# Optimization experiments

Measured on AMD Instinct MI355X. Metric: run time of the kernel, lower is better.

## Reference

```python
import jax, jax.numpy as jnp
import numpy as np

# dimensions
N = 50000    # nodes
E = 600000   # edges
NS = 64      # scalar (0e) channels of node features
NV = 32      # vector (1o) channels of node features
A = 16       # node attr channels (16x0e)
R = 8        # edge embedding dim (radial basis, 8x0e)
H = 8        # fc_hidden_size
AVG_NB = 12.0  # avg_num_neighbors
# gate layout: NS scalars (silu) + NV gate scalars (sigmoid) gating NV vectors
GS = NS + NV  # 96 scalar channels before gate
NW = NS + NS + NV + NV  # 192 per-edge TP weights (paths: s*Y0->0e, s*Y1->1o, v*Y0->1o, v.Y1->0e)


def setup_inputs() -> dict:
    key = jax.random.key(0)
    ks = jax.random.split(key, 20)
    d = {
        'node_s': jax.random.normal(ks[0], (N, NS), jnp.float32),
        'node_v': jax.random.normal(ks[1], (N, NV, 3), jnp.float32),
        'node_attrs': jax.random.normal(ks[2], (N, A), jnp.float32),
        'edge_emb': jax.random.uniform(ks[3], (E, R), jnp.float32),
        'edge_sh0': jnp.ones((E, 1), jnp.float32),
        'edge_sh1': jax.random.normal(ks[4], (E, 3), jnp.float32),
        'edge_index': jax.random.randint(ks[5], (2, E), 0, N),
        # linear_1 on node feats (per-irrep channel mixing)
        'W1s': jax.random.normal(ks[6], (NS, NS), jnp.float32),
        'W1v': jax.random.normal(ks[7], (NV, NV), jnp.float32),
        # radial MLP producing per-edge TP weights
        'Wm1': jax.random.normal(ks[8], (R, H), jnp.float32),
        'Wm2': jax.random.normal(ks[9], (H, NW), jnp.float32),
        # linear_2: TP out (96x0e+96x1o) -> pre-gate (96x0e+32x1o)
        'W2s': jax.random.normal(ks[10], (GS, GS), jnp.float32),
        'W2v': jax.random.normal(ks[11], (NS + NV, NV), jnp.float32),
        # update UVU TP internal weights (msg x attrs)
        'Wt0': jax.random.normal(ks[12], (NS, A), jnp.float32),
        'Wt1': jax.random.normal(ks[13], (NV, A), jnp.float32),
        # linear_3
        'W3s': jax.random.normal(ks[14], (NS, GS), jnp.float32),
        'W3v': jax.random.normal(ks[15], (NV, NV), jnp.float32),
        # self connection: FullyConnectedTensorProduct(node_feats, attrs -> pre-gate)
        'Wsc0': jax.random.normal(ks[16], (NS, A, GS), jnp.float32),
        'Wsc1': jax.random.normal(ks[17], (NV, A, NV), jnp.float32),
    }
    return d


def _gate(s_all, v):
    # s_all: [.., GS]; first NS scalars -> silu, last NV -> sigmoid gates for vectors
    scal = jax.nn.silu(s_all[..., :NS])
    gates = jax.nn.sigmoid(s_all[..., NS:])
    return scal, v * gates[..., None]


def reference(node_s, node_v, node_attrs, edge_emb, edge_sh0, edge_sh1, edge_index,
              W1s, W1v, Wm1, Wm2, W2s, W2v, Wt0, Wt1, W3s, W3v, Wsc0, Wsc1):
    src, dst = edge_index[0], edge_index[1]

    # ---- message ----
    s1 = (node_s @ W1s) / jnp.sqrt(jnp.float32(NS))                       # [N,NS]
    v1 = jnp.einsum('nuc,uv->nvc', node_v, W1v) / jnp.sqrt(jnp.float32(NV))
    ss = s1[src]   # [E,NS]
    vv = v1[src]   # [E,NV,3]

    # per-edge TP weights from radial MLP
    w = jax.nn.silu(edge_emb @ Wm1) @ Wm2                                 # [E,NW]
    w0a, w1a, w1b, w0b = jnp.split(w, [NS, 2 * NS, 2 * NS + NV], axis=1)

    # UVU tensor product with SH edge attrs (lmax=1)
    t0a = w0a * ss * edge_sh0                                             # [E,NS] 0e
    t0b = w0b * jnp.einsum('euc,ec->eu', vv, edge_sh1)                    # [E,NV] 0e
    t1a = w1a[:, :, None] * ss[:, :, None] * edge_sh1[:, None, :]         # [E,NS,3] 1o
    t1b = w1b[:, :, None] * vv * edge_sh0[:, :, None]                     # [E,NV,3] 1o
    tp_s = jnp.concatenate([t0a, t0b], axis=1)                            # [E,96]
    tp_v = jnp.concatenate([t1a, t1b], axis=1)                            # [E,96,3]

    m_s = (tp_s @ W2s) / jnp.sqrt(jnp.float32(GS))                        # [E,GS]
    m_v = jnp.einsum('euc,uv->evc', tp_v, W2v) / jnp.sqrt(jnp.float32(NS + NV))  # [E,NV,3]
    msg_s, msg_v = _gate(m_s, m_v)                                        # [E,NS], [E,NV,3]

    # ---- update ----
    agg_s = jax.ops.segment_sum(msg_s, dst, num_segments=N) / jnp.sqrt(jnp.float32(AVG_NB))
    agg_v = jax.ops.segment_sum(msg_v, dst, num_segments=N) / jnp.sqrt(jnp.float32(AVG_NB))

    u0 = jnp.einsum('nu,na,ua->nu', agg_s, node_attrs, Wt0) / jnp.sqrt(jnp.float32(A))
    u1 = jnp.einsum('nuc,na,ua->nuc', agg_v, node_attrs, Wt1) / jnp.sqrt(jnp.float32(A))

    f_s = (u0 @ W3s) / jnp.sqrt(jnp.float32(NS))                          # [N,GS]
    f_v = jnp.einsum('nuc,uv->nvc', u1, W3v) / jnp.sqrt(jnp.float32(NV))  # [N,NV,3]

    # self connection (fully connected TP with scalar attrs)
    sc_s = jnp.einsum('nu,na,uav->nv', node_s, node_attrs, Wsc0) / jnp.sqrt(jnp.float32(NS * A))
    sc_v = jnp.einsum('nuc,na,uaw->nwc', node_v, node_attrs, Wsc1) / jnp.sqrt(jnp.float32(NV * A))
    f_s = f_s + sc_s
    f_v = f_v + sc_v

    out_s, out_v = _gate(f_s, f_v)                                        # [N,NS], [N,NV,3]
    return jnp.concatenate([out_s, out_v.reshape(N, NV * 3)], axis=1)     # [N,160]
```

## Files before the change

kernel.cpp:

```cpp
#include <hip/hip_runtime.h>
#include <math.h>

#define N 50000
#define E 600000
#define EPB 16
#define LDK 104

typedef __attribute__((ext_vector_type(8))) short short8;
typedef __attribute__((ext_vector_type(4))) float float4v;

__device__ __forceinline__ float silu_f(float x) { return x / (1.f + __expf(-x)); }
__device__ __forceinline__ float sigm_f(float x) { return 1.f / (1.f + __expf(-x)); }
__device__ __forceinline__ unsigned short f2bf(float f) {
  unsigned u = __float_as_uint(f);
  u += 0x7fff + ((u >> 16) & 1);
  return (unsigned short)(u >> 16);
}
__device__ __forceinline__ float bf2f(unsigned short u) {
  return __uint_as_float(((unsigned)u) << 16);
}

__global__ void k_hist(const int* __restrict__ eidx, int* __restrict__ counts) {
  int e = blockIdx.x * 256 + threadIdx.x;
  if (e < E) atomicAdd(&counts[eidx[E + e]], 1);
}

__global__ __launch_bounds__(1024)
void k_scan(const int* __restrict__ counts, int* __restrict__ row_ptr) {
  __shared__ int ssum[1024];
  const int t = threadIdx.x;
  const int CH = 49;
  int lo = t * CH, hi = min(lo + CH, N);
  int s = 0;
  for (int i = lo; i < hi; i++) s += counts[i];
  ssum[t] = s;
  __syncthreads();
  for (int off = 1; off < 1024; off <<= 1) {
    int v = (t >= off) ? ssum[t - off] : 0;
    __syncthreads();
    ssum[t] += v;
    __syncthreads();
  }
  int run = (t == 0) ? 0 : ssum[t - 1];
  for (int i = lo; i < hi; i++) { row_ptr[i] = run; run += counts[i]; }
  if (t == 1023) row_ptr[N] = ssum[1023];
}

__global__ void k_scatter(const int* __restrict__ eidx, const int* __restrict__ row_ptr,
                          int* __restrict__ woff, int* __restrict__ perm) {
  int e = blockIdx.x * 256 + threadIdx.x;
  if (e < E) {
    int d = eidx[E + e];
    int p = atomicAdd(&woff[d], 1);
    perm[row_ptr[d] + p] = e;
  }
}

__global__ void k_prep(const float* __restrict__ Wsc0, const float* __restrict__ W3s,
                       const float* __restrict__ Wsc1, const float* __restrict__ W3v,
                       const float* __restrict__ W2s, const float* __restrict__ W2v,
                       unsigned short* __restrict__ BT, unsigned short* __restrict__ B2T,
                       unsigned short* __restrict__ w2sTg, unsigned short* __restrict__ w2vTg) {
  const float isq96 = 0.10206207261596575f;
  int i = blockIdx.x * 256 + threadIdx.x;
  if (i < 96 * 1088) {
    int j = i / 1088, k = i % 1088;
    float v;
    if (k < 1024) v = Wsc0[(size_t)k * 96 + j] * 0.03125f;
    else          v = W3s[(size_t)(k - 1024) * 96 + j] * 0.125f;
    BT[i] = f2bf(v);
  } else if (i < 96 * 1088 + 32 * 576) {
    int i2 = i - 96 * 1088;
    int w = i2 / 576, k = i2 % 576;
    float v = 0.f;
    if (k < 512)      v = Wsc1[(size_t)k * 32 + w] * 0.04419417382415922f;
    else if (k < 544) v = W3v[(size_t)(k - 512) * 32 + w] * 0.17677669529663689f;
    B2T[i2] = f2bf(v);
  } else if (i < 96 * 1088 + 32 * 576 + 96 * 96) {
    int i3 = i - (96 * 1088 + 32 * 576);
    int j = i3 / 96, k = i3 % 96;
    w2sTg[i3] = f2bf(W2s[(size_t)k * 96 + j] * isq96);
  } else {
    int i4 = i - (96 * 1088 + 32 * 576 + 96 * 96);
    if (i4 < 32 * 96) {
      int v = i4 / 96, u = i4 % 96;
      w2vTg[i4] = f2bf(W2v[(size_t)u * 32 + v] * isq96);
    }
  }
}

__global__ __launch_bounds__(256, 4)
void k_lin1(const float* __restrict__ node_s, const float* __restrict__ node_v,
            const float* __restrict__ W1s, const float* __restrict__ W1v,
            float* __restrict__ s1, float* __restrict__ v1) {
  __shared__ float w1s[64 * 64];
  __shared__ float w1v[32 * 32];
  for (int i = threadIdx.x; i < 64 * 64; i += 256) w1s[i] = W1s[i];
  for (int i = threadIdx.x; i < 32 * 32; i += 256) w1v[i] = W1v[i];
  __syncthreads();
  const float is_ns = 0.125f;
  const float is_nv = 0.17677669529663689f;
  int gtid = blockIdx.x * 256 + threadIdx.x;
  int stride = gridDim.x * 256;
  for (int i = gtid; i < N * 160; i += stride) {
    int n = i / 160, ch = i % 160;
    if (ch < 64) {
      const float* row = node_s + n * 64;
      float acc = 0.f;
#pragma unroll
      for (int u = 0; u < 64; u++) acc += row[u] * w1s[u * 64 + ch];
      s1[n * 64 + ch] = acc * is_ns;
    } else {
      int p = ch - 64, v = p / 3, c = p % 3;
      const float* row = node_v + n * 96;
      float acc = 0.f;
#pragma unroll
      for (int u = 0; u < 32; u++) acc += row[u * 3 + c] * w1v[u * 32 + v];
      v1[n * 96 + p] = acc * is_nv;
    }
  }
}

template<int STORE>
__global__ __launch_bounds__(256, 4)
void k_msg(const float* __restrict__ s1, const float* __restrict__ v1,
           const float* __restrict__ emb, const float* __restrict__ sh0g,
           const float* __restrict__ sh1g, const int* __restrict__ eidx,
           const float* __restrict__ Wm1, const float* __restrict__ Wm2,
           const unsigned short* __restrict__ w2sTg, const unsigned short* __restrict__ w2vTg,
           float* __restrict__ aggs, float* __restrict__ aggv,
           unsigned short* __restrict__ msgS, unsigned short* __restrict__ msgV) {
  __shared__ float wm2s[192 * 9];
  __shared__ float wm1s[64];
  __shared__ unsigned short tps[EPB * LDK];
  __shared__ unsigned short tpv[EPB * 3 * LDK];
  __shared__ float gat[EPB][33];
  __shared__ float hb[EPB][8];
  __shared__ float sh1b[EPB][4];
  __shared__ float sh0b[EPB];
  __shared__ int ssrc[EPB];
  __shared__ int sdst[EPB];

  const int t = threadIdx.x;
  const int wave = t >> 6, lane = t & 63;
  const int lm = lane & 15, quad = lane >> 4;
  const int subc = t & 15;

  for (int i = t; i < 192 * 8; i += 256) {
    int h = i / 192, c = i % 192;
    wm2s[c * 9 + h] = Wm2[i];
  }
  if (t < 64) wm1s[t] = Wm1[t];

  short8 b1fr[2][3], b2fr[3];
  {
    const int nt0 = wave;
    const int nt1 = (wave + 4 < 6) ? wave + 4 : wave;
    const int nv2 = wave & 1;
#pragma unroll
    for (int kk = 0; kk < 3; kk++) {
      b1fr[0][kk] = *(const short8*)&w2sTg[(nt0 * 16 + lm) * 96 + kk * 32 + quad * 8];
      b1fr[1][kk] = *(const short8*)&w2sTg[(nt1 * 16 + lm) * 96 + kk * 32 + quad * 8];
      b2fr[kk]    = *(const short8*)&w2vTg[(nv2 * 16 + lm) * 96 + kk * 32 + quad * 8];
    }
  }
  __syncthreads();

  for (int pass = blockIdx.x; pass < E / EPB; pass += gridDim.x) {
    const int ebase = pass * EPB;
    __syncthreads();
    if (t < EPB) {
      ssrc[t] = eidx[ebase + t];
      if (!STORE) sdst[t] = eidx[E + ebase + t];
      sh0b[t] = sh0g[ebase + t];
    } else if (t >= 64 && t < 64 + EPB * 3) {
      int i = t - 64;
      sh1b[i / 3][i % 3] = sh1g[ebase * 3 + i];
    } else if (t >= 128) {
      int i = t - 128, el = i >> 3, sub = i & 7;
      float acc = 0.f;
#pragma unroll
      for (int r = 0; r < 8; r++) acc += emb[(ebase + el) * 8 + r] * wm1s[r * 8 + sub];
      hb[el][sub] = silu_f(acc);
    }
    __syncthreads();
    {
      const int el = t >> 4, sub = subc;
      const int src = ssrc[el];
      const float s0v = sh0b[el];
      const float x0 = sh1b[el][0], x1 = sh1b[el][1], x2 = sh1b[el][2];
      float hr[8];
#pragma unroll
      for (int h = 0; h < 8; h++) hr[h] = hb[el][h];
      const float4v ss = *(const float4v*)&s1[(size_t)src * 64 + sub * 4];
      unsigned short tsv[4], tvv[3][4];
#pragma unroll
      for (int i = 0; i < 4; i++) {
        float w0a = 0.f, w1a = 0.f;
#pragma unroll
        for (int h = 0; h < 8; h++) {
          w0a += hr[h] * wm2s[(sub * 4 + i) * 9 + h];
          w1a += hr[h] * wm2s[(64 + sub * 4 + i) * 9 + h];
        }
        const float ssu = ss[i];
        tsv[i] = f2bf(w0a * ssu * s0v);
        const float base = w1a * ssu;
        tvv[0][i] = f2bf(base * x0);
        tvv[1][i] = f2bf(base * x1);
        tvv[2][i] = f2bf(base * x2);
      }
      *(uint2*)&tps[el * LDK + sub * 4] = *(uint2*)tsv;
#pragma unroll
      for (int c = 0; c < 3; c++)
        *(uint2*)&tpv[(el * 3 + c) * LDK + sub * 4] = *(uint2*)tvv[c];
      const float2* vp = (const float2*)&v1[(size_t)src * 96 + sub * 6];
      const float2 va = vp[0], vb = vp[1], vc = vp[2];
      const float v6[6] = {va.x, va.y, vb.x, vb.y, vc.x, vc.y};
      unsigned short ts2[2], tv2[3][2];
#pragma unroll
      for (int i2 = 0; i2 < 2; i2++) {
        float w1b = 0.f, w0b = 0.f;
#pragma unroll
        for (int h = 0; h < 8; h++) {
          w1b += hr[h] * wm2s[(128 + sub * 2 + i2) * 9 + h];
          w0b += hr[h] * wm2s[(160 + sub * 2 + i2) * 9 + h];
        }
        const float vx = v6[i2 * 3 + 0], vy = v6[i2 * 3 + 1], vz = v6[i2 * 3 + 2];
        ts2[i2] = f2bf(w0b * (vx * x0 + vy * x1 + vz * x2));
        tv2[0][i2] = f2bf(w1b * vx * s0v);
        tv2[1][i2] = f2bf(w1b * vy * s0v);
        tv2[2][i2] = f2bf(w1b * vz * s0v);
      }
      *(unsigned*)&tps[el * LDK + 64 + sub * 2] = *(unsigned*)ts2;
#pragma unroll
      for (int c = 0; c < 3; c++)
        *(unsigned*)&tpv[(el * 3 + c) * LDK + 64 + sub * 2] = *(unsigned*)tv2[c];
    }
    __syncthreads();
    {
      short8 afr[3];
#pragma unroll
      for (int kk = 0; kk < 3; kk++)
        afr[kk] = *(const short8*)&tps[lm * LDK + kk * 32 + quad * 8];
#pragma unroll
      for (int t2 = 0; t2 < 2; t2++) {
        const int nt = wave + t2 * 4;
        if (nt < 6) {
          float4v acc = {0.f, 0.f, 0.f, 0.f};
#pragma unroll
          for (int kk = 0; kk < 3; kk++)
            acc = __builtin_amdgcn_mfma_f32_16x16x32_bf16(afr[kk], b1fr[t2][kk], acc, 0, 0, 0);
          const int j = nt * 16 + lm;
#pragma unroll
          for (int reg = 0; reg < 4; reg++) {
            const int e = quad * 4 + reg;
            const float val = acc[reg];
            if (j < 64) {
              if (STORE) msgS[(size_t)(ebase + e) * 64 + j] = f2bf(silu_f(val));
              else atomicAdd(&aggs[(size_t)sdst[e] * 64 + j], silu_f(val));
            } else {
              gat[e][j - 64] = sigm_f(val);
            }
          }
        }
      }
    }
    __syncthreads();
#pragma unroll
    for (int t2 = 0; t2 < 2; t2++) {
      const int tile = wave + t2 * 4;
      if (tile < 6) {
        const int mt = tile >> 1, nt2 = tile & 1;
        float4v acc = {0.f, 0.f, 0.f, 0.f};
#pragma unroll
        for (int kk = 0; kk < 3; kk++) {
          short8 a = *(const short8*)&tpv[(mt * 16 + lm) * LDK + kk * 32 + quad * 8];
          acc = __builtin_amdgcn_mfma_f32_16x16x32_bf16(a, b2fr[kk], acc, 0, 0, 0);
        }
        const int v = nt2 * 16 + lm;
#pragma unroll
        for (int reg = 0; reg < 4; reg++) {
          const int r = mt * 16 + quad * 4 + reg;
          const int e = (r * 171) >> 9, c = r - 3 * e;
          const float val = acc[reg] * gat[e][v];
          if (STORE) msgV[(size_t)(ebase + e) * 96 + v * 3 + c] = f2bf(val);
          else atomicAdd(&aggv[(size_t)sdst[e] * 96 + v * 3 + c], val);
        }
      }
    }
  }
}

__global__ __launch_bounds__(256, 8)
void k_agg(const unsigned short* __restrict__ msgS, const unsigned short* __restrict__ msgV,
           const int* __restrict__ rowp, const int* __restrict__ perm,
           float* __restrict__ aggs, float* __restrict__ aggv) {
  const int wv = threadIdx.x >> 6, lane = threadIdx.x & 63;
  const int n = blockIdx.x * 4 + wv;
  const int lo = rowp[n], hi = rowp[n + 1];
  float sS = 0.f, v0 = 0.f, v1a = 0.f;
  int r = lo;
  for (; r + 2 <= hi; r += 2) {
    const int e0 = perm[r], e1 = perm[r + 1];
    const unsigned short a0 = msgS[(size_t)e0 * 64 + lane];
    const unsigned short a1 = msgS[(size_t)e1 * 64 + lane];
    const unsigned short b0 = msgV[(size_t)e0 * 96 + lane];
    const unsigned short b1 = msgV[(size_t)e1 * 96 + lane];
    unsigned short c0 = 0, c1 = 0;
    if (lane < 32) {
      c0 = msgV[(size_t)e0 * 96 + 64 + lane];
      c1 = msgV[(size_t)e1 * 96 + 64 + lane];
    }
    sS += bf2f(a0) + bf2f(a1);
    v0 += bf2f(b0) + bf2f(b1);
    v1a += bf2f(c0) + bf2f(c1);
  }
  for (; r < hi; r++) {
    const int e0 = perm[r];
    sS += bf2f(msgS[(size_t)e0 * 64 + lane]);
    v0 += bf2f(msgV[(size_t)e0 * 96 + lane]);
    if (lane < 32) v1a += bf2f(msgV[(size_t)e0 * 96 + 64 + lane]);
  }
  aggs[(size_t)n * 64 + lane] = sS;
  aggv[(size_t)n * 96 + lane] = v0;
  if (lane < 32) aggv[(size_t)n * 96 + 64 + lane] = v1a;
}

__global__ __launch_bounds__(256, 4)
void k_c1(const float* __restrict__ node_s, const float* __restrict__ attrs,
          const float* __restrict__ aggs, const float* __restrict__ Wt0,
          const unsigned short* __restrict__ BT,
          float* __restrict__ out, float* __restrict__ gates) {
  __shared__ float s_row[32][64];
  __shared__ float attr[32][16];
  __shared__ float t0[32][64];
  __shared__ float wt0[1024];
  __shared__ unsigned short As[32 * 72];
  const int t = threadIdx.x;
  const int wave = t >> 6, lane = t & 63, lm = lane & 15, quad = lane >> 4;
  const int nbase = blockIdx.x * 32;

  for (int i = t; i < 1024; i += 256) wt0[i] = Wt0[i];
  for (int i = t; i < 2048; i += 256) {
    int nl = i >> 6, u = i & 63, n = nbase + nl;
    s_row[nl][u] = (n < N) ? node_s[(size_t)n * 64 + u] : 0.f;
    t0[nl][u]    = (n < N) ? aggs[(size_t)n * 64 + u] : 0.f;
  }
  for (int i = t; i < 512; i += 256) {
    int nl = i >> 4, a = i & 15, n = nbase + nl;
    attr[nl][a] = (n < N) ? attrs[(size_t)n * 16 + a] : 0.f;
  }
  __syncthreads();
  for (int i = t; i < 2048; i += 256) {
    int nl = i >> 6, u = i & 63;
    float d0 = 0.f;
#pragma unroll
    for (int a = 0; a < 16; a++) d0 += attr[nl][a] * wt0[u * 16 + a];
    t0[nl][u] *= d0 * 0.07216878364870322f;
  }

  float4v acc[3] = {{0,0,0,0},{0,0,0,0},{0,0,0,0}};
  int mts[3], nts[3];
#pragma unroll
  for (int tt = 0; tt < 3; tt++) {
    const int tile = wave + tt * 4;
    mts[tt] = tile / 6;
    nts[tt] = tile % 6;
  }

  for (int kc = 0; kc < 17; kc++) {
    __syncthreads();
    {
      const int row = t >> 3, c0 = (t & 7) * 8;
      unsigned short tmp[8];
      if (kc < 16) {
        const int u = kc * 4 + (c0 >> 4);
        const float sval = s_row[row][u];
        const int ab = c0 & 8;
#pragma unroll
        for (int i = 0; i < 8; i++) tmp[i] = f2bf(sval * attr[row][ab + i]);
      } else {
#pragma unroll
        for (int i = 0; i < 8; i++) tmp[i] = f2bf(t0[row][c0 + i]);
      }
      *(uint4*)&As[row * 72 + c0] = *(uint4*)tmp;
    }
    __syncthreads();
#pragma unroll
    for (int ks = 0; ks < 2; ks++) {
      short8 am0 = *(const short8*)&As[(lm) * 72 + ks * 32 + quad * 8];
      short8 am1 = *(const short8*)&As[(16 + lm) * 72 + ks * 32 + quad * 8];
#pragma unroll
      for (int tt = 0; tt < 3; tt++) {
        short8 b = *(const short8*)&BT[(size_t)(nts[tt] * 16 + lm) * 1088 + kc * 64 + ks * 32 + quad * 8];
        acc[tt] = __builtin_amdgcn_mfma_f32_16x16x32_bf16(mts[tt] ? am1 : am0, b, acc[tt], 0, 0, 0);
      }
    }
  }
#pragma unroll
  for (int tt = 0; tt < 3; tt++) {
    const int j = nts[tt] * 16 + lm;
#pragma unroll
    for (int reg = 0; reg < 4; reg++) {
      const int m = mts[tt] * 16 + quad * 4 + reg;
      const int n = nbase + m;
      if (n < N) {
        const float val = acc[tt][reg];
        if (j < 64) out[(size_t)n * 160 + j] = silu_f(val);
        else        gates[(size_t)n * 32 + (j - 64)] = sigm_f(val);
      }
    }
  }
}

__global__ __launch_bounds__(256, 3)
void k_c2(const float* __restrict__ node_v, const float* __restrict__ attrs,
          const float* __restrict__ aggv, const float* __restrict__ Wt1,
          const unsigned short* __restrict__ B2T, const float* __restrict__ gts,
          float* __restrict__ out) {
  __shared__ float nvs[32][96];
  __shared__ float t1s[32][96];
  __shared__ float attr[32][16];
  __shared__ float wt1[512];
  __shared__ unsigned short As2[96 * 72];
  const int t = threadIdx.x;
  const int wave = t >> 6, lane = t & 63, lm = lane & 15, quad = lane >> 4;
  const int nbase = blockIdx.x * 32;

  for (int i = t; i < 512; i += 256) wt1[i] = Wt1[i];
  for (int i = t; i < 32 * 96; i += 256) {
    int nl = i / 96, rr = i % 96, n = nbase + nl;
    nvs[nl][rr] = (n < N) ? node_v[(size_t)n * 96 + rr] : 0.f;
    t1s[nl][rr] = (n < N) ? aggv[(size_t)n * 96 + rr] : 0.f;
  }
  for (int i = t; i < 512; i += 256) {
    int nl = i >> 4, a = i & 15, n = nbase + nl;
    attr[nl][a] = (n < N) ? attrs[(size_t)n * 16 + a] : 0.f;
  }
  __syncthreads();
  for (int i = t; i < 1024; i += 256) {
    int nl = i >> 5, u = i & 31;
    float d1 = 0.f;
#pragma unroll
    for (int a = 0; a < 16; a++) d1 += attr[nl][a] * wt1[u * 16 + a];
    d1 *= 0.07216878364870322f;
    t1s[nl][u * 3 + 0] *= d1; t1s[nl][u * 3 + 1] *= d1; t1s[nl][u * 3 + 2] *= d1;
  }

  float4v acc[3] = {{0,0,0,0},{0,0,0,0},{0,0,0,0}};
  int mts[3], nts[3];
#pragma unroll
  for (int tt = 0; tt < 3; tt++) {
    const int tile = wave + tt * 4;
    mts[tt] = tile >> 1;
    nts[tt] = tile & 1;
  }

  for (int kc = 0; kc < 9; kc++) {
    __syncthreads();
#pragma unroll
    for (int jj = 0; jj < 3; jj++) {
      const int job = t + jj * 256;
      const int row = job >> 3, c0 = (job & 7) * 8;
      const int nl = (row * 171) >> 9, c = row - 3 * nl;
      const int kbase = kc * 64 + c0;
      unsigned short tmp[8];
      if (kbase < 512) {
        const int u = kbase >> 4;
        const float vval = nvs[nl][u * 3 + c];
        const int ab = c0 & 8;
#pragma unroll
        for (int i = 0; i < 8; i++) tmp[i] = f2bf(vval * attr[nl][ab + i]);
      } else if (kbase < 544) {
        const int u2 = kbase - 512;
#pragma unroll
        for (int i = 0; i < 8; i++) tmp[i] = f2bf(t1s[nl][(u2 + i) * 3 + c]);
      } else {
#pragma unroll
        for (int i = 0; i < 8; i++) tmp[i] = 0;
      }
      *(uint4*)&As2[row * 72 + c0] = *(uint4*)tmp;
    }
    __syncthreads();
#pragma unroll
    for (int ks = 0; ks < 2; ks++) {
#pragma unroll
      for (int tt = 0; tt < 3; tt++) {
        short8 a = *(const short8*)&As2[(mts[tt] * 16 + lm) * 72 + ks * 32 + quad * 8];
        short8 b = *(const short8*)&B2T[(size_t)(nts[tt] * 16 + lm) * 576 + kc * 64 + ks * 32 + quad * 8];
        acc[tt] = __builtin_amdgcn_mfma_f32_16x16x32_bf16(a, b, acc[tt], 0, 0, 0);
      }
    }
  }
#pragma unroll
  for (int tt = 0; tt < 3; tt++) {
    const int w = nts[tt] * 16 + lm;
#pragma unroll
    for (int reg = 0; reg < 4; reg++) {
      const int row = mts[tt] * 16 + quad * 4 + reg;
      const int nl = (row * 171) >> 9, c = row - 3 * nl;
      const int n = nbase + nl;
      if (n < N)
        out[(size_t)n * 160 + 64 + w * 3 + c] = acc[tt][reg] * gts[(size_t)n * 32 + w];
    }
  }
}

extern "C" void kernel_launch(void* const* d_in, const int* in_sizes, int n_in,
                              void* d_out, int out_size, void* d_ws, size_t ws_size,
                              hipStream_t stream) {
  const float* node_s = (const float*)d_in[0];
  const float* node_v = (const float*)d_in[1];
  const float* attrs  = (const float*)d_in[2];
  const float* emb    = (const float*)d_in[3];
  const float* sh0    = (const float*)d_in[4];
  const float* sh1    = (const float*)d_in[5];
  const int*   eidx   = (const int*)d_in[6];
  const float* W1s    = (const float*)d_in[7];
  const float* W1v    = (const float*)d_in[8];
  const float* Wm1    = (const float*)d_in[9];
  const float* Wm2    = (const float*)d_in[10];
  const float* W2s    = (const float*)d_in[11];
  const float* W2v    = (const float*)d_in[12];
  const float* Wt0    = (const float*)d_in[13];
  const float* Wt1    = (const float*)d_in[14];
  const float* W3s    = (const float*)d_in[15];
  const float* W3v    = (const float*)d_in[16];
  const float* Wsc0   = (const float*)d_in[17];
  const float* Wsc1   = (const float*)d_in[18];

  char* p = (char*)d_ws;
  float* s1  = (float*)p;  p += (size_t)N * 64 * 4;
  float* v1f = (float*)p;  p += (size_t)N * 96 * 4;
  float* gts = (float*)p;  p += (size_t)N * 32 * 4;
  unsigned short* BT    = (unsigned short*)p;  p += (size_t)96 * 1088 * 2;
  unsigned short* B2T   = (unsigned short*)p;  p += (size_t)32 * 576 * 2;
  unsigned short* w2sTg = (unsigned short*)p;  p += (size_t)96 * 96 * 2;
  unsigned short* w2vTg = (unsigned short*)p;  p += (size_t)32 * 96 * 2;
  char* pmode = p;
  size_t base = (size_t)(pmode - (char*)d_ws);
  size_t need_store = base + ((size_t)N + 1) * 4 + (size_t)N * 4 + (size_t)N * 4
                    + (size_t)E * 4 + (size_t)E * 64 * 2 + (size_t)E * 96 * 2;
  const bool store = (ws_size >= need_store);

  k_prep<<<528, 256, 0, stream>>>(Wsc0, W3s, Wsc1, W3v, W2s, W2v, BT, B2T, w2sTg, w2vTg);
  k_lin1<<<1024, 256, 0, stream>>>(node_s, node_v, W1s, W1v, s1, v1f);

  if (store) {
    int* rowp = (int*)pmode;
    int* cnt  = rowp + (N + 1);
    int* woff = cnt + N;
    int* perm = woff + N;
    unsigned short* msgS = (unsigned short*)(perm + E);
    unsigned short* msgV = msgS + (size_t)E * 64;
    hipMemsetAsync(cnt, 0, (size_t)N * 2 * 4, stream);
    k_hist<<<(E + 255) / 256, 256, 0, stream>>>(eidx, cnt);
    k_scan<<<1, 1024, 0, stream>>>(cnt, rowp);
    k_scatter<<<(E + 255) / 256, 256, 0, stream>>>(eidx, rowp, woff, perm);
    k_msg<1><<<1536, 256, 0, stream>>>(s1, v1f, emb, sh0, sh1, eidx, Wm1, Wm2,
                                       w2sTg, w2vTg, nullptr, nullptr, msgS, msgV);
    float* aggs = s1;
    float* aggv = v1f;
    k_agg<<<N / 4, 256, 0, stream>>>(msgS, msgV, rowp, perm, aggs, aggv);
    k_c1<<<1563, 256, 0, stream>>>(node_s, attrs, aggs, Wt0, BT, (float*)d_out, gts);
    k_c2<<<1563, 256, 0, stream>>>(node_v, attrs, aggv, Wt1, B2T, gts, (float*)d_out);
  } else {
    float* aggs = (float*)pmode;
    float* aggv = aggs + (size_t)N * 64;
    hipMemsetAsync(aggs, 0, (size_t)N * 160 * 4, stream);
    k_msg<0><<<1536, 256, 0, stream>>>(s1, v1f, emb, sh0, sh1, eidx, Wm1, Wm2,
                                       w2sTg, w2vTg, aggs, aggv, nullptr, nullptr);
    k_c1<<<1563, 256, 0, stream>>>(node_s, attrs, aggs, Wt0, BT, (float*)d_out, gts);
    k_c2<<<1563, 256, 0, stream>>>(node_v, attrs, aggv, Wt1, B2T, gts, (float*)d_out);
  }
}
```

Baseline: 779.3 us.

## Process edges in destination-sorted order so aggregation reads messages contiguously

The message kernel now walks edges through the destination-sorted permutation and writes each message at its sorted position. The aggregation kernel can then read messages sequentially per node instead of gathering through perm. In exchange, the per-edge inputs (src index, sh0, sh1, edge embedding) are now read through an indirection and are gathered rather than streamed. The message kernel grid is also cut from 1536 to 1024 blocks.

```diff
diff --git a/kernel.cpp b/kernel.cpp
--- a/kernel.cpp
+++ b/kernel.cpp
@@ -126,6 +126,7 @@
 void k_msg(const float* __restrict__ s1, const float* __restrict__ v1,
            const float* __restrict__ emb, const float* __restrict__ sh0g,
            const float* __restrict__ sh1g, const int* __restrict__ eidx,
+           const int* __restrict__ perm,
            const float* __restrict__ Wm1, const float* __restrict__ Wm2,
            const unsigned short* __restrict__ w2sTg, const unsigned short* __restrict__ w2vTg,
            float* __restrict__ aggs, float* __restrict__ aggv,
@@ -170,17 +171,21 @@
     const int ebase = pass * EPB;
     __syncthreads();
     if (t < EPB) {
-      ssrc[t] = eidx[ebase + t];
+      const int e = STORE ? perm[ebase + t] : (ebase + t);
+      ssrc[t] = eidx[e];
       if (!STORE) sdst[t] = eidx[E + ebase + t];
-      sh0b[t] = sh0g[ebase + t];
+      sh0b[t] = sh0g[e];
     } else if (t >= 64 && t < 64 + EPB * 3) {
       int i = t - 64;
-      sh1b[i / 3][i % 3] = sh1g[ebase * 3 + i];
+      const int el = i / 3, c = i % 3;
+      const int e = STORE ? perm[ebase + el] : (ebase + el);
+      sh1b[el][c] = sh1g[e * 3 + c];
     } else if (t >= 128) {
       int i = t - 128, el = i >> 3, sub = i & 7;
+      const int e = STORE ? perm[ebase + el] : (ebase + el);
       float acc = 0.f;
 #pragma unroll
-      for (int r = 0; r < 8; r++) acc += emb[(ebase + el) * 8 + r] * wm1s[r * 8 + sub];
+      for (int r = 0; r < 8; r++) acc += emb[e * 8 + r] * wm1s[r * 8 + sub];
       hb[el][sub] = silu_f(acc);
     }
     __syncthreads();
@@ -293,7 +298,7 @@
 
 __global__ __launch_bounds__(256, 8)
 void k_agg(const unsigned short* __restrict__ msgS, const unsigned short* __restrict__ msgV,
-           const int* __restrict__ rowp, const int* __restrict__ perm,
+           const int* __restrict__ rowp,
            float* __restrict__ aggs, float* __restrict__ aggv) {
   const int wv = threadIdx.x >> 6, lane = threadIdx.x & 63;
   const int n = blockIdx.x * 4 + wv;
@@ -301,25 +306,23 @@
   float sS = 0.f, v0 = 0.f, v1a = 0.f;
   int r = lo;
   for (; r + 2 <= hi; r += 2) {
-    const int e0 = perm[r], e1 = perm[r + 1];
-    const unsigned short a0 = msgS[(size_t)e0 * 64 + lane];
-    const unsigned short a1 = msgS[(size_t)e1 * 64 + lane];
-    const unsigned short b0 = msgV[(size_t)e0 * 96 + lane];
-    const unsigned short b1 = msgV[(size_t)e1 * 96 + lane];
+    const unsigned short a0 = msgS[(size_t)r * 64 + lane];
+    const unsigned short a1 = msgS[(size_t)(r + 1) * 64 + lane];
+    const unsigned short b0 = msgV[(size_t)r * 96 + lane];
+    const unsigned short b1 = msgV[(size_t)(r + 1) * 96 + lane];
     unsigned short c0 = 0, c1 = 0;
     if (lane < 32) {
-      c0 = msgV[(size_t)e0 * 96 + 64 + lane];
-      c1 = msgV[(size_t)e1 * 96 + 64 + lane];
+      c0 = msgV[(size_t)r * 96 + 64 + lane];
+      c1 = msgV[(size_t)(r + 1) * 96 + 64 + lane];
     }
     sS += bf2f(a0) + bf2f(a1);
     v0 += bf2f(b0) + bf2f(b1);
     v1a += bf2f(c0) + bf2f(c1);
   }
   for (; r < hi; r++) {
-    const int e0 = perm[r];
-    sS += bf2f(msgS[(size_t)e0 * 64 + lane]);
-    v0 += bf2f(msgV[(size_t)e0 * 96 + lane]);
-    if (lane < 32) v1a += bf2f(msgV[(size_t)e0 * 96 + 64 + lane]);
+    sS += bf2f(msgS[(size_t)r * 64 + lane]);
+    v0 += bf2f(msgV[(size_t)r * 96 + lane]);
+    if (lane < 32) v1a += bf2f(msgV[(size_t)r * 96 + 64 + lane]);
   }
   aggs[(size_t)n * 64 + lane] = sS;
   aggv[(size_t)n * 96 + lane] = v0;
@@ -557,18 +560,18 @@
     k_hist<<<(E + 255) / 256, 256, 0, stream>>>(eidx, cnt);
     k_scan<<<1, 1024, 0, stream>>>(cnt, rowp);
     k_scatter<<<(E + 255) / 256, 256, 0, stream>>>(eidx, rowp, woff, perm);
-    k_msg<1><<<1536, 256, 0, stream>>>(s1, v1f, emb, sh0, sh1, eidx, Wm1, Wm2,
+    k_msg<1><<<1024, 256, 0, stream>>>(s1, v1f, emb, sh0, sh1, eidx, perm, Wm1, Wm2,
                                        w2sTg, w2vTg, nullptr, nullptr, msgS, msgV);
     float* aggs = s1;
     float* aggv = v1f;
-    k_agg<<<N / 4, 256, 0, stream>>>(msgS, msgV, rowp, perm, aggs, aggv);
+    k_agg<<<N / 4, 256, 0, stream>>>(msgS, msgV, rowp, aggs, aggv);
     k_c1<<<1563, 256, 0, stream>>>(node_s, attrs, aggs, Wt0, BT, (float*)d_out, gts);
     k_c2<<<1563, 256, 0, stream>>>(node_v, attrs, aggv, Wt1, B2T, gts, (float*)d_out);
   } else {
     float* aggs = (float*)pmode;
     float* aggv = aggs + (size_t)N * 64;
     hipMemsetAsync(aggs, 0, (size_t)N * 160 * 4, stream);
-    k_msg<0><<<1536, 256, 0, stream>>>(s1, v1f, emb, sh0, sh1, eidx, Wm1, Wm2,
+    k_msg<0><<<1024, 256, 0, stream>>>(s1, v1f, emb, sh0, sh1, eidx, nullptr, Wm1, Wm2,
                                        w2sTg, w2vTg, aggs, aggv, nullptr, nullptr);
     k_c1<<<1563, 256, 0, stream>>>(node_s, attrs, aggs, Wt0, BT, (float*)d_out, gts);
     k_c2<<<1563, 256, 0, stream>>>(node_v, attrs, aggv, Wt1, B2T, gts, (float*)d_out);
```

After: 740.4 us. -5.0%, faster.
